# Performance work log

Measured on AMD Instinct MI355X. Metric: run time of the kernel, lower is better.

Reference implementation:

```python
import jax, jax.numpy as jnp
import numpy as np

NUM_CLASSES = 14
ATTN_DIM = 64
BN_EPS = 1e-5

def setup_inputs() -> dict:
    key = jax.random.key(0)
    ks = jax.random.split(key, 6)
    B, F = 16384, 2048
    C, D = NUM_CLASSES, ATTN_DIM
    std = 0.02
    return {
        "features": jax.random.normal(ks[0], (B, F), jnp.float32),
        "W_proj": jax.random.normal(ks[1], (F, F), jnp.float32) * std,
        "b_proj": jnp.zeros((F,), jnp.float32),
        "bn_gamma": jnp.ones((F,), jnp.float32),
        "bn_beta": jnp.zeros((F,), jnp.float32),
        "W_qk": jax.random.normal(ks[2], (C * 2 * D, F), jnp.float32) * std,
        "gamma": jax.random.normal(ks[3], (C,), jnp.float32) * 0.1,
        "W_fc": jax.random.normal(ks[4], (C, F), jnp.float32) * std,
        "b_fc": jnp.zeros((C,), jnp.float32),
    }

def reference(features, W_proj, b_proj, bn_gamma, bn_beta, W_qk, gamma, W_fc, b_fc):
    B = features.shape[0]
    C, D = NUM_CLASSES, ATTN_DIM
    # fc logits
    logits = features @ W_fc.T + b_fc  # [B, C]
    # projection: Linear -> BatchNorm1d (training-mode batch stats) -> ReLU
    h = features @ W_proj.T + b_proj  # [B, P]
    mu = jnp.mean(h, axis=0)
    var = jnp.var(h, axis=0)  # biased, as torch BN uses for normalization
    h = (h - mu) * jax.lax.rsqrt(var + BN_EPS) * bn_gamma + bn_beta
    h = jax.nn.relu(h)
    # per-class q, k
    qk = h @ W_qk.T  # [B, 2*C*D]
    q, k = jnp.split(qk, 2, axis=-1)
    q = q.reshape(B, C, D)
    k = k.reshape(B, C, D)
    attn = jnp.einsum("bcd,bed->bce", q, k)  # [B, C, C]
    diag = jnp.diagonal(attn, axis1=-2, axis2=-1)  # [B, C]
    attn = attn - diag[..., None]
    attn = attn / jnp.max(jnp.abs(attn), axis=-1, keepdims=True)
    corr = jnp.einsum("bce,be->bc", attn, jax.nn.sigmoid(logits))  # [B, C]
    return logits + gamma * corr
```

## Files before the change

kernel.cpp:

```cpp
#include <hip/hip_runtime.h>
#include <stdint.h>

#define BROWS 16384
#define FDIM  2048
#define NCLS  14
#define ADIM  64
#define NCAT  2176
#define QKN   1792

typedef __attribute__((ext_vector_type(8))) short bhalf8_t;
typedef __attribute__((ext_vector_type(4))) float f32x4_t;

__device__ __forceinline__ unsigned short f2bf(float f) {
  unsigned int u = __builtin_bit_cast(unsigned int, f);
  u += 0x7fffu + ((u >> 16) & 1u);
  return (unsigned short)(u >> 16);
}
__device__ __forceinline__ float bf2f(unsigned short s) {
  return __builtin_bit_cast(float, (unsigned int)s << 16);
}

__device__ __forceinline__ void gl_lds16(const void* g, void* l) {
  __builtin_amdgcn_global_load_lds(
      (const __attribute__((address_space(1))) unsigned int*)g,
      (__attribute__((address_space(3))) unsigned int*)l, 16, 0, 0);
}


__global__ void cast8_bf16(const float* __restrict__ src,
                           unsigned short* __restrict__ dst, int n8) {
  int t = blockIdx.x * 256 + threadIdx.x;
  if (t >= n8) return;
  const float4* s = (const float4*)src + 2 * (size_t)t;
  float4 a = s[0], b = s[1];
  bhalf8_t o;
  o[0] = f2bf(a.x); o[1] = f2bf(a.y); o[2] = f2bf(a.z); o[3] = f2bf(a.w);
  o[4] = f2bf(b.x); o[5] = f2bf(b.y); o[6] = f2bf(b.z); o[7] = f2bf(b.w);
  *((bhalf8_t*)dst + t) = o;
}

__global__ void build_wcat(const float* __restrict__ Wp, const float* __restrict__ Wf,
                           unsigned short* __restrict__ dst) {
  int row = blockIdx.x;
  int c8 = threadIdx.x * 8;
  const float* src = nullptr;
  if (row < 2048) src = Wp + (size_t)row * FDIM + c8;
  else if (row < 2048 + NCLS) src = Wf + (size_t)(row - 2048) * FDIM + c8;
  bhalf8_t o = {0,0,0,0,0,0,0,0};
  if (src) {
    float4 a = *(const float4*)src, b = *(const float4*)(src + 4);
    o[0] = f2bf(a.x); o[1] = f2bf(a.y); o[2] = f2bf(a.z); o[3] = f2bf(a.w);
    o[4] = f2bf(b.x); o[5] = f2bf(b.y); o[6] = f2bf(b.z); o[7] = f2bf(b.w);
  }
  *(bhalf8_t*)(dst + (size_t)row * FDIM + c8) = o;
}

template<int MODE>
__global__ __launch_bounds__(256) void gemm_bt(
    const unsigned short* __restrict__ A, const unsigned short* __restrict__ Bw,
    const float* __restrict__ bp, const float* __restrict__ bfc,
    unsigned short* __restrict__ Cb, float* __restrict__ logits,
    float* __restrict__ colsum, float* __restrict__ colsq,
    int K, int lda, int ldb, int ldc)
{
  __shared__ unsigned short lA[128 * 64];
  __shared__ unsigned short lB[128 * 64];
  const int tid = threadIdx.x;
  const int lane = tid & 63, wv = tid >> 6;
  const int m = lane & 15, quad = lane >> 4;
  const size_t rowBase = (size_t)blockIdx.x * 128;
  const size_t colBase = (size_t)blockIdx.y * 128;
  const int m0 = (wv >> 1) * 64, n0 = (wv & 1) * 64;

  f32x4_t acc[4][4];
#pragma unroll
  for (int i = 0; i < 4; ++i)
#pragma unroll
    for (int j = 0; j < 4; ++j) acc[i][j] = (f32x4_t){0.f, 0.f, 0.f, 0.f};

  int sS[4];
  size_t gA[4], gB[4];
#pragma unroll
  for (int i = 0; i < 4; ++i) {
    int s = ((i * 4 + wv) << 6) + lane;
    int r = s >> 3, qp = s & 7;
    int q = qp ^ (r & 7);
    sS[i] = s;
    gA[i] = (rowBase + r) * (size_t)lda + q * 8;
    gB[i] = (colBase + r) * (size_t)ldb + q * 8;
  }

  for (int kb = 0; kb < K; kb += 64) {
#pragma unroll
    for (int i = 0; i < 4; ++i) {
      gl_lds16(A + gA[i] + kb, &lA[sS[i] * 8]);
      gl_lds16(Bw + gB[i] + kb, &lB[sS[i] * 8]);
    }
    __syncthreads();
#pragma unroll
    for (int ks = 0; ks < 2; ++ks) {
      const int qc = ks * 4 + quad;
      bhalf8_t af[4], bf[4];
#pragma unroll
      for (int mi = 0; mi < 4; ++mi) {
        int r = m0 + mi * 16 + m;
        af[mi] = *(const bhalf8_t*)&lA[(r * 8 + (qc ^ (r & 7))) * 8];
      }
#pragma unroll
      for (int ni = 0; ni < 4; ++ni) {
        int r = n0 + ni * 16 + m;
        bf[ni] = *(const bhalf8_t*)&lB[(r * 8 + (qc ^ (r & 7))) * 8];
      }
#pragma unroll
      for (int mi = 0; mi < 4; ++mi)
#pragma unroll
        for (int ni = 0; ni < 4; ++ni)
          acc[mi][ni] = __builtin_amdgcn_mfma_f32_16x16x32_bf16(af[mi], bf[ni], acc[mi][ni], 0, 0, 0);
    }
    __syncthreads();
  }

  if (MODE == 0) {
    if (colBase < 2048) {
#pragma unroll
      for (int ni = 0; ni < 4; ++ni) {
        int gcol = (int)colBase + n0 + ni * 16 + m;
        float bv = bp[gcol];
        float s = 0.f, q = 0.f;
#pragma unroll
        for (int mi = 0; mi < 4; ++mi) {
          size_t grow = rowBase + m0 + mi * 16 + quad * 4;
#pragma unroll
          for (int r = 0; r < 4; ++r) {
            float v = acc[mi][ni][r] + bv;
            Cb[(grow + r) * (size_t)ldc + gcol] = f2bf(v);
            s += v; q += v * v;
          }
        }
        s += __shfl_xor(s, 16, 64); s += __shfl_xor(s, 32, 64);
        q += __shfl_xor(q, 16, 64); q += __shfl_xor(q, 32, 64);
        if (quad == 0) { atomicAdd(&colsum[gcol], s); atomicAdd(&colsq[gcol], q); }
      }
    } else if (n0 == 0) {
      float bv = (m < NCLS) ? bfc[m] : 0.f;
#pragma unroll
      for (int mi = 0; mi < 4; ++mi) {
        size_t grow = rowBase + m0 + mi * 16 + quad * 4;
#pragma unroll
        for (int r = 0; r < 4; ++r)
          logits[(grow + r) * 16 + m] = acc[mi][0][r] + bv;
      }
    }
  } else {
#pragma unroll
    for (int ni = 0; ni < 4; ++ni) {
      int gcol = (int)colBase + n0 + ni * 16 + m;
#pragma unroll
      for (int mi = 0; mi < 4; ++mi) {
        size_t grow = rowBase + m0 + mi * 16 + quad * 4;
#pragma unroll
        for (int r = 0; r < 4; ++r)
          Cb[(grow + r) * (size_t)ldc + gcol] = f2bf(acc[mi][ni][r]);
      }
    }
  }
}


__global__ void bn_finalize(const float* __restrict__ cs, const float* __restrict__ cq,
                            const float* __restrict__ g, const float* __restrict__ bt,
                            float* __restrict__ scale, float* __restrict__ shift) {
  int c = blockIdx.x * 256 + threadIdx.x;
  if (c >= FDIM) return;
  const float inv = 1.f / (float)BROWS;
  float mu = cs[c] * inv;
  float var = cq[c] * inv - mu * mu;
  float sc = g[c] * rsqrtf(var + 1e-5f);
  scale[c] = sc;
  shift[c] = bt[c] - mu * sc;
}

__global__ void bn_apply(unsigned short* __restrict__ hb, const float* __restrict__ sc,
                         const float* __restrict__ sh) {
  int t = blockIdx.x * 256 + threadIdx.x;
  int row = t >> 8;
  int c8 = (t & 255) << 3;
  unsigned short* p = hb + (size_t)row * FDIM + c8;
  bhalf8_t v = *(bhalf8_t*)p;
  float4 s0 = *(const float4*)(sc + c8), s1 = *(const float4*)(sc + c8 + 4);
  float4 h0 = *(const float4*)(sh + c8), h1 = *(const float4*)(sh + c8 + 4);
  bhalf8_t o;
  o[0] = f2bf(fmaxf(bf2f((unsigned short)v[0]) * s0.x + h0.x, 0.f));
  o[1] = f2bf(fmaxf(bf2f((unsigned short)v[1]) * s0.y + h0.y, 0.f));
  o[2] = f2bf(fmaxf(bf2f((unsigned short)v[2]) * s0.z + h0.z, 0.f));
  o[3] = f2bf(fmaxf(bf2f((unsigned short)v[3]) * s0.w + h0.w, 0.f));
  o[4] = f2bf(fmaxf(bf2f((unsigned short)v[4]) * s1.x + h1.x, 0.f));
  o[5] = f2bf(fmaxf(bf2f((unsigned short)v[5]) * s1.y + h1.y, 0.f));
  o[6] = f2bf(fmaxf(bf2f((unsigned short)v[6]) * s1.z + h1.z, 0.f));
  o[7] = f2bf(fmaxf(bf2f((unsigned short)v[7]) * s1.w + h1.w, 0.f));
  *(bhalf8_t*)p = o;
}

__global__ __launch_bounds__(256) void attn_ep(
    const unsigned short* __restrict__ qk, const float* __restrict__ logits,
    const float* __restrict__ gamma, float* __restrict__ out)
{
  const int lane = threadIdx.x & 63;
  const int wv = threadIdx.x >> 6;
  const int b = blockIdx.x * 4 + wv;
  const int m = lane & 15, quad = lane >> 4;
  const unsigned short* qrow = qk + (size_t)b * QKN;
  f32x4_t acc = (f32x4_t){0.f, 0.f, 0.f, 0.f};
#pragma unroll
  for (int ks = 0; ks < 2; ++ks) {
    bhalf8_t af = {0,0,0,0,0,0,0,0}, bf = {0,0,0,0,0,0,0,0};
    if (m < NCLS) {
      af = *(const bhalf8_t*)(qrow + m * 64 + ks * 32 + quad * 8);
      bf = *(const bhalf8_t*)(qrow + 896 + m * 64 + ks * 32 + quad * 8);
    }
    acc = __builtin_amdgcn_mfma_f32_16x16x32_bf16(af, bf, acc, 0, 0, 0);
  }
  float logit_e = (m < NCLS) ? logits[(size_t)b * 16 + m] : 0.f;
  float sig = 1.f / (1.f + __expf(-logit_e));
  float corr[4];
#pragma unroll
  for (int r = 0; r < 4; ++r) {
    int c = quad * 4 + r;
    float diag = __shfl(acc[r], (lane & 48) + c, 64);
    float a = acc[r] - diag;
    float av = (m < NCLS) ? fabsf(a) : 0.f;
    av = fmaxf(av, __shfl_xor(av, 1, 64));
    av = fmaxf(av, __shfl_xor(av, 2, 64));
    av = fmaxf(av, __shfl_xor(av, 4, 64));
    av = fmaxf(av, __shfl_xor(av, 8, 64));
    float v = (m < NCLS) ? (a / av) * sig : 0.f;
    v += __shfl_xor(v, 1, 64);
    v += __shfl_xor(v, 2, 64);
    v += __shfl_xor(v, 4, 64);
    v += __shfl_xor(v, 8, 64);
    corr[r] = v;
  }
  if (m == 0) {
#pragma unroll
    for (int r = 0; r < 4; ++r) {
      int c = quad * 4 + r;
      if (c < NCLS) {
        float lc = logits[(size_t)b * 16 + c];
        out[(size_t)b * NCLS + c] = lc + gamma[c] * corr[r];
      }
    }
  }
}


extern "C" void kernel_launch(void* const* d_in, const int* in_sizes, int n_in,
                              void* d_out, int out_size, void* d_ws, size_t ws_size,
                              hipStream_t stream) {
  const float* features = (const float*)d_in[0];
  const float* W_proj   = (const float*)d_in[1];
  const float* b_proj   = (const float*)d_in[2];
  const float* bn_gamma = (const float*)d_in[3];
  const float* bn_beta  = (const float*)d_in[4];
  const float* W_qk     = (const float*)d_in[5];
  const float* gamma    = (const float*)d_in[6];
  const float* W_fc     = (const float*)d_in[7];
  const float* b_fc     = (const float*)d_in[8];
  float* out = (float*)d_out;

  char* ws = (char*)d_ws;
  unsigned short* featC   = (unsigned short*)ws;
  unsigned short* hbuf    = (unsigned short*)(ws + 67108864);
  unsigned short* WcatC   = (unsigned short*)(ws + 134217728);
  unsigned short* WqkC    = (unsigned short*)(ws + 143130624);
  unsigned short* qkC     = (unsigned short*)(ws + 150470656);
  float*          logitsB = (float*)(ws + 209190912);
  float*          colsum  = (float*)(ws + 210239488);
  float*          colsq   = (float*)(ws + 210247680);
  float*          scalev  = (float*)(ws + 210255872);
  float*          shiftv  = (float*)(ws + 210264064);

  hipMemsetAsync(colsum, 0, 16384, stream);

  cast8_bf16<<<16384, 256, 0, stream>>>(features, featC, (BROWS * FDIM) / 8);
  build_wcat<<<NCAT, 256, 0, stream>>>(W_proj, W_fc, WcatC);
  cast8_bf16<<<1792, 256, 0, stream>>>(W_qk, WqkC, (QKN * FDIM) / 8);

  gemm_bt<0><<<dim3(BROWS / 128, NCAT / 128), 256, 0, stream>>>(
      featC, WcatC, b_proj, b_fc, hbuf, logitsB, colsum, colsq,
      FDIM, FDIM, FDIM, FDIM);

  bn_finalize<<<8, 256, 0, stream>>>(colsum, colsq, bn_gamma, bn_beta, scalev, shiftv);
  bn_apply<<<16384, 256, 0, stream>>>(hbuf, scalev, shiftv);

  gemm_bt<1><<<dim3(BROWS / 128, QKN / 128), 256, 0, stream>>>(
      hbuf, WqkC, nullptr, nullptr, qkC, nullptr, nullptr, nullptr,
      FDIM, FDIM, FDIM, QKN);

  attn_ep<<<BROWS / 4, 256, 0, stream>>>(qkC, logitsB, gamma, out);
}
```

Baseline: 622.7 us.

## Replace 128x128 GEMM with 256x256 double-buffered ping-pong pipelined kernel

Both bf16 GEMMs now use a 512-thread, 256x256 output-tile kernel. LDS is double buffered, with global-to-LDS loads issued in four sub-stages interleaved with MFMA phases, separated by barriers and s_setprio. Workgroups are remapped for L2 locality, and B rows are clamped so the 2176-column concat matrix fits 9 column tiles. The aim is more reuse per byte loaded and overlap of memory with matrix math, at the cost of more registers, more LDS, and waste in the last, mostly padded column tile of the first GEMM.

```diff
diff --git a/kernel.cpp b/kernel.cpp
--- a/kernel.cpp
+++ b/kernel.cpp
@@ -25,6 +25,12 @@
       (const __attribute__((address_space(1))) unsigned int*)g,
       (__attribute__((address_space(3))) unsigned int*)l, 16, 0, 0);
 }
+
+#define BAR() do { \
+    asm volatile("" ::: "memory"); \
+    __builtin_amdgcn_s_barrier(); \
+    asm volatile("" ::: "memory"); \
+  } while (0)
 
 
 __global__ void cast8_bf16(const float* __restrict__ src,
@@ -55,97 +61,190 @@
   *(bhalf8_t*)(dst + (size_t)row * FDIM + c8) = o;
 }
 
+
 template<int MODE>
-__global__ __launch_bounds__(256) void gemm_bt(
+__global__ __launch_bounds__(512, 2) void gemm256_bt(
     const unsigned short* __restrict__ A, const unsigned short* __restrict__ Bw,
     const float* __restrict__ bp, const float* __restrict__ bfc,
     unsigned short* __restrict__ Cb, float* __restrict__ logits,
     float* __restrict__ colsum, float* __restrict__ colsq,
-    int K, int lda, int ldb, int ldc)
+    int K, int lda, int ldb, int ldc, int nBr)
 {
-  __shared__ unsigned short lA[128 * 64];
-  __shared__ unsigned short lB[128 * 64];
-  const int tid = threadIdx.x;
-  const int lane = tid & 63, wv = tid >> 6;
+  __shared__ unsigned short L[2][2][2][8192];
+
+  const int t = threadIdx.x;
+  const int lane = t & 63;
+  const int wv = t >> 6;
   const int m = lane & 15, quad = lane >> 4;
-  const size_t rowBase = (size_t)blockIdx.x * 128;
-  const size_t colBase = (size_t)blockIdx.y * 128;
-  const int m0 = (wv >> 1) * 64, n0 = (wv & 1) * 64;
-
-  f32x4_t acc[4][4];
-#pragma unroll
-  for (int i = 0; i < 4; ++i)
+  const int wm = wv >> 2, wn = wv & 3;
+
+  const int nwg = gridDim.x;
+  const int wg = ((blockIdx.x & 7) * (nwg >> 3)) + (blockIdx.x >> 3);
+  const int bx = wg & 63;
+  const int by = wg >> 6;
+  const int rowBase = bx << 8;
+  const int colBase = by << 8;
+
+  const int bO = (wn & 1) << 12;
+  const int ofs0 = m * 64 + ((quad ^ (m & 7)) << 3);
+  const int ofs1 = ofs0 ^ 32;
+
+  const int r0 = t >> 3;
+  const int q8 = ((t ^ r0) & 7) << 3;
+  const int ldD = t << 3;
+  const unsigned int aOff =
+      (unsigned int)(rowBase + r0) * (unsigned int)lda + (unsigned int)q8;
+  unsigned int bOff00, bOff01, bOff10, bOff11;
+  {
+    int rr;
+    rr = colBase + r0;        if (rr > nBr - 1) rr = nBr - 1;
+    bOff00 = (unsigned int)rr * (unsigned int)ldb + q8;
+    rr = colBase + 64 + r0;   if (rr > nBr - 1) rr = nBr - 1;
+    bOff01 = (unsigned int)rr * (unsigned int)ldb + q8;
+    rr = colBase + 128 + r0;  if (rr > nBr - 1) rr = nBr - 1;
+    bOff10 = (unsigned int)rr * (unsigned int)ldb + q8;
+    rr = colBase + 192 + r0;  if (rr > nBr - 1) rr = nBr - 1;
+    bOff11 = (unsigned int)rr * (unsigned int)ldb + q8;
+  }
+
+#define STAGEA0(b, kb) do { \
+    gl_lds16(A + aOff + (unsigned int)(kb), &L[b][0][0][ldD]); \
+    gl_lds16(A + aOff + (unsigned int)(64 * lda) + (unsigned int)(kb), &L[b][0][0][ldD + 4096]); \
+  } while (0)
+#define STAGEA1(b, kb) do { \
+    gl_lds16(A + aOff + (unsigned int)(128 * lda) + (unsigned int)(kb), &L[b][0][1][ldD]); \
+    gl_lds16(A + aOff + (unsigned int)(192 * lda) + (unsigned int)(kb), &L[b][0][1][ldD + 4096]); \
+  } while (0)
+#define STAGEB0(b, kb) do { \
+    gl_lds16(Bw + bOff00 + (unsigned int)(kb), &L[b][1][0][ldD]); \
+    gl_lds16(Bw + bOff01 + (unsigned int)(kb), &L[b][1][0][ldD + 4096]); \
+  } while (0)
+#define STAGEB1(b, kb) do { \
+    gl_lds16(Bw + bOff10 + (unsigned int)(kb), &L[b][1][1][ldD]); \
+    gl_lds16(Bw + bOff11 + (unsigned int)(kb), &L[b][1][1][ldD + 4096]); \
+  } while (0)
+
+#define RDA(v, roff) \
+    v##_0 = *(const bhalf8_t*)&LA[(roff) + ofs0]; \
+    v##_1 = *(const bhalf8_t*)&LA[(roff) + ofs1];
+#define RDB(v, roff) \
+    v##_0 = *(const bhalf8_t*)&LB[(roff) + ofs0]; \
+    v##_1 = *(const bhalf8_t*)&LB[(roff) + ofs1];
+#define MM(i, j, av, bv) \
+    acc[i][j] = __builtin_amdgcn_mfma_f32_16x16x32_bf16(av##_0, bv##_0, acc[i][j], 0, 0, 0); \
+    acc[i][j] = __builtin_amdgcn_mfma_f32_16x16x32_bf16(av##_1, bv##_1, acc[i][j], 0, 0, 0);
+
+  f32x4_t acc[8][4];
+#pragma unroll
+  for (int i = 0; i < 8; ++i)
 #pragma unroll
     for (int j = 0; j < 4; ++j) acc[i][j] = (f32x4_t){0.f, 0.f, 0.f, 0.f};
 
-  int sS[4];
-  size_t gA[4], gB[4];
-#pragma unroll
-  for (int i = 0; i < 4; ++i) {
-    int s = ((i * 4 + wv) << 6) + lane;
-    int r = s >> 3, qp = s & 7;
-    int q = qp ^ (r & 7);
-    sS[i] = s;
-    gA[i] = (rowBase + r) * (size_t)lda + q * 8;
-    gB[i] = (colBase + r) * (size_t)ldb + q * 8;
-  }
-
-  for (int kb = 0; kb < K; kb += 64) {
-#pragma unroll
-    for (int i = 0; i < 4; ++i) {
-      gl_lds16(A + gA[i] + kb, &lA[sS[i] * 8]);
-      gl_lds16(Bw + gB[i] + kb, &lB[sS[i] * 8]);
-    }
-    __syncthreads();
-#pragma unroll
-    for (int ks = 0; ks < 2; ++ks) {
-      const int qc = ks * 4 + quad;
-      bhalf8_t af[4], bf[4];
-#pragma unroll
-      for (int mi = 0; mi < 4; ++mi) {
-        int r = m0 + mi * 16 + m;
-        af[mi] = *(const bhalf8_t*)&lA[(r * 8 + (qc ^ (r & 7))) * 8];
-      }
-#pragma unroll
-      for (int ni = 0; ni < 4; ++ni) {
-        int r = n0 + ni * 16 + m;
-        bf[ni] = *(const bhalf8_t*)&lB[(r * 8 + (qc ^ (r & 7))) * 8];
-      }
-#pragma unroll
-      for (int mi = 0; mi < 4; ++mi)
-#pragma unroll
-        for (int ni = 0; ni < 4; ++ni)
-          acc[mi][ni] = __builtin_amdgcn_mfma_f32_16x16x32_bf16(af[mi], bf[ni], acc[mi][ni], 0, 0, 0);
-    }
-    __syncthreads();
-  }
+  const int NT = K >> 6;
+
+  STAGEA0(0, 0);
+  STAGEA1(0, 0);
+  STAGEB0(0, 0);
+  STAGEB1(0, 0);
+  {
+    const int kb1 = (NT > 1) ? 64 : 0;
+    STAGEB0(1, kb1);
+    STAGEB1(1, kb1);
+  }
+  asm volatile("s_waitcnt vmcnt(4)" ::: "memory");
+  BAR();
+
+  for (int u = 0; u < NT; ++u) {
+    const int buf = u & 1;
+    const unsigned short* LA = &L[buf][0][wm][0];
+    const unsigned short* LB = &L[buf][1][wn >> 1][bO];
+    const int kbA = (u + 1 < NT) ? (u + 1) << 6 : 0;
+    const int kbB = (u + 2 < NT) ? (u + 2) << 6 : 0;
+
+    bhalf8_t a0_0, a0_1, a1_0, a1_1, a2_0, a2_1, a3_0, a3_1;
+    bhalf8_t b0_0, b0_1, b1_0, b1_1, b2_0, b2_1, b3_0, b3_1;
+
+    RDA(a0, 0);     RDA(a1, 1024);  RDA(a2, 2048);  RDA(a3, 3072);
+    RDB(b0, 0);     RDB(b1, 1024);
+    if (buf) { STAGEA0(0, kbA); } else { STAGEA0(1, kbA); }
+    BAR();
+    __builtin_amdgcn_s_setprio(1);
+    MM(0, 0, a0, b0); MM(0, 1, a0, b1);
+    MM(1, 0, a1, b0); MM(1, 1, a1, b1);
+    MM(2, 0, a2, b0); MM(2, 1, a2, b1);
+    MM(3, 0, a3, b0); MM(3, 1, a3, b1);
+    __builtin_amdgcn_s_setprio(0);
+    BAR();
+
+    RDB(b2, 2048);  RDB(b3, 3072);
+    if (buf) { STAGEA1(0, kbA); } else { STAGEA1(1, kbA); }
+    BAR();
+    __builtin_amdgcn_s_setprio(1);
+    MM(0, 2, a0, b2); MM(0, 3, a0, b3);
+    MM(1, 2, a1, b2); MM(1, 3, a1, b3);
+    MM(2, 2, a2, b2); MM(2, 3, a2, b3);
+    MM(3, 2, a3, b2); MM(3, 3, a3, b3);
+    __builtin_amdgcn_s_setprio(0);
+    BAR();
+
+    RDA(a0, 4096);  RDA(a1, 5120);  RDA(a2, 6144);  RDA(a3, 7168);
+    if (buf) { STAGEB0(1, kbB); } else { STAGEB0(0, kbB); }
+    BAR();
+    __builtin_amdgcn_s_setprio(1);
+    MM(4, 0, a0, b0); MM(4, 1, a0, b1);
+    MM(5, 0, a1, b0); MM(5, 1, a1, b1);
+    MM(6, 0, a2, b0); MM(6, 1, a2, b1);
+    MM(7, 0, a3, b0); MM(7, 1, a3, b1);
+    __builtin_amdgcn_s_setprio(0);
+    BAR();
+
+    if (buf) { STAGEB1(1, kbB); } else { STAGEB1(0, kbB); }
+    BAR();
+    __builtin_amdgcn_s_setprio(1);
+    MM(4, 2, a0, b2); MM(4, 3, a0, b3);
+    MM(5, 2, a1, b2); MM(5, 3, a1, b3);
+    MM(6, 2, a2, b2); MM(6, 3, a2, b3);
+    MM(7, 2, a3, b2); MM(7, 3, a3, b3);
+    __builtin_amdgcn_s_setprio(0);
+    asm volatile("s_waitcnt vmcnt(4)" ::: "memory");
+    BAR();
+  }
+  asm volatile("s_waitcnt vmcnt(0)" ::: "memory");
+
+#undef STAGEA0
+#undef STAGEA1
+#undef STAGEB0
+#undef STAGEB1
+#undef RDA
+#undef RDB
+#undef MM
 
   if (MODE == 0) {
     if (colBase < 2048) {
 #pragma unroll
       for (int ni = 0; ni < 4; ++ni) {
-        int gcol = (int)colBase + n0 + ni * 16 + m;
-        float bv = bp[gcol];
-        float s = 0.f, q = 0.f;
-#pragma unroll
-        for (int mi = 0; mi < 4; ++mi) {
-          size_t grow = rowBase + m0 + mi * 16 + quad * 4;
+        const int gcol = colBase + wn * 64 + ni * 16 + m;
+        const float bv = bp[gcol];
+        float s = 0.f, qq = 0.f;
+#pragma unroll
+        for (int mi = 0; mi < 8; ++mi) {
+          const size_t grow = (size_t)(rowBase + wm * 128 + mi * 16 + quad * 4);
 #pragma unroll
           for (int r = 0; r < 4; ++r) {
             float v = acc[mi][ni][r] + bv;
             Cb[(grow + r) * (size_t)ldc + gcol] = f2bf(v);
-            s += v; q += v * v;
+            s += v; qq += v * v;
           }
         }
         s += __shfl_xor(s, 16, 64); s += __shfl_xor(s, 32, 64);
-        q += __shfl_xor(q, 16, 64); q += __shfl_xor(q, 32, 64);
-        if (quad == 0) { atomicAdd(&colsum[gcol], s); atomicAdd(&colsq[gcol], q); }
+        qq += __shfl_xor(qq, 16, 64); qq += __shfl_xor(qq, 32, 64);
+        if (quad == 0) { atomicAdd(&colsum[gcol], s); atomicAdd(&colsq[gcol], qq); }
       }
-    } else if (n0 == 0) {
-      float bv = (m < NCLS) ? bfc[m] : 0.f;
-#pragma unroll
-      for (int mi = 0; mi < 4; ++mi) {
-        size_t grow = rowBase + m0 + mi * 16 + quad * 4;
+    } else if (wn == 0) {
+      const float bv = (m < NCLS) ? bfc[m] : 0.f;
+#pragma unroll
+      for (int mi = 0; mi < 8; ++mi) {
+        const size_t grow = (size_t)(rowBase + wm * 128 + mi * 16 + quad * 4);
 #pragma unroll
         for (int r = 0; r < 4; ++r)
           logits[(grow + r) * 16 + m] = acc[mi][0][r] + bv;
@@ -154,10 +253,10 @@
   } else {
 #pragma unroll
     for (int ni = 0; ni < 4; ++ni) {
-      int gcol = (int)colBase + n0 + ni * 16 + m;
-#pragma unroll
-      for (int mi = 0; mi < 4; ++mi) {
-        size_t grow = rowBase + m0 + mi * 16 + quad * 4;
+      const int gcol = colBase + wn * 64 + ni * 16 + m;
+#pragma unroll
+      for (int mi = 0; mi < 8; ++mi) {
+        const size_t grow = (size_t)(rowBase + wm * 128 + mi * 16 + quad * 4);
 #pragma unroll
         for (int r = 0; r < 4; ++r)
           Cb[(grow + r) * (size_t)ldc + gcol] = f2bf(acc[mi][ni][r]);
@@ -285,16 +384,16 @@
   build_wcat<<<NCAT, 256, 0, stream>>>(W_proj, W_fc, WcatC);
   cast8_bf16<<<1792, 256, 0, stream>>>(W_qk, WqkC, (QKN * FDIM) / 8);
 
-  gemm_bt<0><<<dim3(BROWS / 128, NCAT / 128), 256, 0, stream>>>(
+  gemm256_bt<0><<<576, 512, 0, stream>>>(
       featC, WcatC, b_proj, b_fc, hbuf, logitsB, colsum, colsq,
-      FDIM, FDIM, FDIM, FDIM);
+      FDIM, FDIM, FDIM, FDIM, NCAT);
 
   bn_finalize<<<8, 256, 0, stream>>>(colsum, colsq, bn_gamma, bn_beta, scalev, shiftv);
   bn_apply<<<16384, 256, 0, stream>>>(hbuf, scalev, shiftv);
 
-  gemm_bt<1><<<dim3(BROWS / 128, QKN / 128), 256, 0, stream>>>(
+  gemm256_bt<1><<<448, 512, 0, stream>>>(
       hbuf, WqkC, nullptr, nullptr, qkC, nullptr, nullptr, nullptr,
-      FDIM, FDIM, FDIM, QKN);
+      FDIM, FDIM, FDIM, QKN, QKN);
 
   attn_ep<<<BROWS / 4, 256, 0, stream>>>(qkC, logitsB, gamma, out);
 }
```

Result: faster. 573.9 us (-7.8%).
